# Optimization experiments

Hardware: AMD Instinct MI355X
Metric: run time of the kernel (lower is better)

## Reference

```python
import jax, jax.numpy as jnp
import numpy as np


def setup_inputs() -> dict:
    key = jax.random.key(0)
    k1, k2 = jax.random.split(key)
    num_tokens, top_k, num_experts = 1048576, 8, 64
    top_scores = jax.random.uniform(k1, (num_tokens, top_k), dtype=jnp.float32)
    selected_experts_indices = jax.random.randint(
        k2, (num_tokens, top_k), 0, num_experts, dtype=jnp.int64
    ) if jax.config.jax_enable_x64 else jax.random.randint(
        k2, (num_tokens, top_k), 0, num_experts, dtype=jnp.int32
    )
    return {
        "top_scores": top_scores,
        "selected_experts_indices": selected_experts_indices,
        "num_experts": num_experts,
    }


def reference(top_scores, selected_experts_indices, num_experts):
    flat_idx = selected_experts_indices.reshape(-1)  # [num_tokens*top_k]
    # histogram of tokens per expert (torch.histc returns float)
    num_tokens_per_expert = jnp.bincount(flat_idx, length=num_experts).astype(jnp.float32)
    # stable argsort by expert id -> permutation grouping tokens by expert
    token_indices_experts_sorted = jnp.argsort(flat_idx, stable=True)
    # gather routing scores into expert-sorted order
    top_scores_experts_sorted = top_scores.reshape(-1)[token_indices_experts_sorted]
    return (
        top_scores_experts_sorted,
        token_indices_experts_sorted,
        num_tokens_per_expert,
    )
```

## Files before the change

### kernel.cpp

```cpp
#include <hip/hip_runtime.h>


#define TILE 2048
#define WCH  512
#define RND  8

__device__ __forceinline__ unsigned long long match_mask(
    unsigned key,
    unsigned long long b0, unsigned long long b1, unsigned long long b2,
    unsigned long long b3, unsigned long long b4, unsigned long long b5,
    unsigned long long am) {
  unsigned long long m = am;
  m &= (key & 1u)  ? b0 : ~b0;
  m &= (key & 2u)  ? b1 : ~b1;
  m &= (key & 4u)  ? b2 : ~b2;
  m &= (key & 8u)  ? b3 : ~b3;
  m &= (key & 16u) ? b4 : ~b4;
  m &= (key & 32u) ? b5 : ~b5;
  return m;
}

__global__ __launch_bounds__(256) void hist_kernel(
    const int* __restrict__ idx, unsigned* __restrict__ countsT,
    int N, int nb) {
  __shared__ unsigned h[4][64];
  const int wave = threadIdx.x >> 6;
  const int lane = threadIdx.x & 63;

  long long base = (long long)blockIdx.x * TILE;
  long long rem = (long long)N - base;
  unsigned cnt = 0;

  if (rem >= TILE) {
    const int4* v = (const int4*)(idx + base);
    int4 x0 = v[threadIdx.x];
    int4 x1 = v[threadIdx.x + 256];
    unsigned es[8] = {
        ((unsigned)x0.x) & 63u, ((unsigned)x0.y) & 63u,
        ((unsigned)x0.z) & 63u, ((unsigned)x0.w) & 63u,
        ((unsigned)x1.x) & 63u, ((unsigned)x1.y) & 63u,
        ((unsigned)x1.z) & 63u, ((unsigned)x1.w) & 63u};
    #pragma unroll
    for (int r = 0; r < 8; ++r) {
      unsigned e = es[r];
      unsigned long long b0 = __ballot(e & 1u);
      unsigned long long b1 = __ballot(e & 2u);
      unsigned long long b2 = __ballot(e & 4u);
      unsigned long long b3 = __ballot(e & 8u);
      unsigned long long b4 = __ballot(e & 16u);
      unsigned long long b5 = __ballot(e & 32u);
      cnt += (unsigned)__popcll(
          match_mask((unsigned)lane, b0, b1, b2, b3, b4, b5, ~0ull));
    }
  } else {
    long long wstart = base + (long long)wave * WCH;
    for (int r = 0; r < RND; ++r) {
      long long i = wstart + (long long)r * 64 + lane;
      bool valid = i < (long long)N;
      unsigned long long am = __ballot(valid ? 1 : 0);
      unsigned e = valid ? (((unsigned)idx[i]) & 63u) : 0u;
      unsigned long long b0 = __ballot(e & 1u);
      unsigned long long b1 = __ballot(e & 2u);
      unsigned long long b2 = __ballot(e & 4u);
      unsigned long long b3 = __ballot(e & 8u);
      unsigned long long b4 = __ballot(e & 16u);
      unsigned long long b5 = __ballot(e & 32u);
      cnt += (unsigned)__popcll(
          match_mask((unsigned)lane, b0, b1, b2, b3, b4, b5, am));
    }
  }

  h[wave][lane] = cnt;
  __syncthreads();
  if (threadIdx.x < 64) {
    countsT[(size_t)blockIdx.x * 64 + threadIdx.x] =
        h[0][threadIdx.x] + h[1][threadIdx.x] + h[2][threadIdx.x] + h[3][threadIdx.x];
  }
}

__global__ __launch_bounds__(256) void scan_kernel(
    unsigned* __restrict__ countsT, unsigned* __restrict__ totals,
    float* __restrict__ out_counts, int nb) {
  int e = blockIdx.x;
  int t = threadIdx.x;
  int per = (nb + 255) >> 8;
  int base = t * per;

  unsigned s = 0;
  for (int j = 0; j < per; ++j) {
    int w = base + j;
    if (w < nb) s += countsT[(size_t)w * 64 + e];
  }
  __shared__ unsigned sh[256];
  sh[t] = s;
  __syncthreads();
  for (int d = 1; d < 256; d <<= 1) {
    unsigned v = sh[t];
    unsigned a = (t >= d) ? sh[t - d] : 0u;
    __syncthreads();
    sh[t] = v + a;
    __syncthreads();
  }
  unsigned incl = sh[t];
  unsigned run = incl - s;
  for (int j = 0; j < per; ++j) {
    int w = base + j;
    if (w < nb) {
      unsigned v = countsT[(size_t)w * 64 + e];
      countsT[(size_t)w * 64 + e] = run;
      run += v;
    }
  }
  if (t == 255) {
    totals[e] = incl;
    out_counts[e] = (float)incl;
  }
}

__global__ __launch_bounds__(256, 8) void scatter_kernel(
    const int* __restrict__ idx, const float* __restrict__ scores,
    const unsigned* __restrict__ baseT, const unsigned* __restrict__ totals,
    float* __restrict__ out_scores, float* __restrict__ out_idx,
    int N, int nb) {
  __shared__ uint2    sdat[TILE];
  __shared__ unsigned shc[4][64];
  __shared__ unsigned gdest[64];

  const int wave = threadIdx.x >> 6;
  const int lane = threadIdx.x & 63;
  const unsigned long long lt = (1ull << lane) - 1ull;

  const long long start = (long long)blockIdx.x * TILE + (long long)wave * WCH;
  const bool fullt = ((long long)(blockIdx.x + 1) * TILE) <= (long long)N;

  const unsigned tot = totals[lane];
  const unsigned gb0 = baseT[(size_t)blockIdx.x * 64 + lane];

  unsigned e_pk[2] = {0, 0};
  unsigned r_pk[2] = {0, 0};
  unsigned c_pk[2] = {0, 0};
  float    sreg[RND];
  unsigned wtotal = 0;

  if (fullt) {
    #pragma unroll
    for (int r = 0; r < RND; ++r) {
      long long i = start + r * 64 + lane;
      unsigned e = ((unsigned)idx[i]) & 63u;
      sreg[r] = scores[i];
      unsigned long long b0 = __ballot(e & 1u);
      unsigned long long b1 = __ballot(e & 2u);
      unsigned long long b2 = __ballot(e & 4u);
      unsigned long long b3 = __ballot(e & 8u);
      unsigned long long b4 = __ballot(e & 16u);
      unsigned long long b5 = __ballot(e & 32u);
      unsigned long long ms = match_mask(e, b0, b1, b2, b3, b4, b5, ~0ull);
      unsigned rank = (unsigned)__popcll(ms & lt);
      unsigned cnt  = (unsigned)__popcll(
          match_mask((unsigned)lane, b0, b1, b2, b3, b4, b5, ~0ull));
      const int q = r >> 2, sh = (r & 3) * 8;
      e_pk[q] |= e << sh;
      r_pk[q] |= rank << sh;
      c_pk[q] |= cnt << sh;
      wtotal += cnt;
    }
  } else {
    for (int j = threadIdx.x; j < TILE; j += 256) sdat[j].y = 0xFFFFFFFFu;
    __syncthreads();
    for (int r = 0; r < RND; ++r) {
      long long i = start + (long long)r * 64 + lane;
      bool valid = i < (long long)N;
      unsigned long long am = __ballot(valid ? 1 : 0);
      unsigned e = valid ? (((unsigned)idx[i]) & 63u) : 0u;
      sreg[r] = valid ? scores[i] : 0.0f;
      unsigned long long b0 = __ballot(e & 1u);
      unsigned long long b1 = __ballot(e & 2u);
      unsigned long long b2 = __ballot(e & 4u);
      unsigned long long b3 = __ballot(e & 8u);
      unsigned long long b4 = __ballot(e & 16u);
      unsigned long long b5 = __ballot(e & 32u);
      unsigned long long ms = match_mask(e, b0, b1, b2, b3, b4, b5, am);
      unsigned rank = (unsigned)__popcll(ms & lt);
      unsigned cnt  = (unsigned)__popcll(
          match_mask((unsigned)lane, b0, b1, b2, b3, b4, b5, am));
      const int q = r >> 2, sh = (r & 3) * 8;
      e_pk[q] |= e << sh;
      r_pk[q] |= rank << sh;
      c_pk[q] |= cnt << sh;
      wtotal += cnt;
    }
  }

  shc[wave][lane] = wtotal;
  __syncthreads();

  unsigned c0 = shc[0][lane], c1 = shc[1][lane];
  unsigned c2 = shc[2][lane], c3 = shc[3][lane];
  unsigned bt = c0 + c1 + c2 + c3;
  unsigned wpre = 0;
  if (wave > 0) wpre += c0;
  if (wave > 1) wpre += c1;
  if (wave > 2) wpre += c2;

  unsigned s = bt;
  #pragma unroll
  for (int d = 1; d < 64; d <<= 1) {
    unsigned nv = __shfl_up(s, d, 64);
    if (lane >= d) s += nv;
  }
  unsigned bstart = s - bt;
  unsigned wbase = bstart + wpre;

  unsigned cur[RND];
  {
    unsigned acc = wbase;
    #pragma unroll
    for (int r = 0; r < RND; ++r) {
      cur[r] = acc;
      acc += (c_pk[r >> 2] >> ((r & 3) * 8)) & 0xffu;
    }
  }

  if (wave == 0) {
    unsigned s2 = tot;
    #pragma unroll
    for (int d = 1; d < 64; d <<= 1) {
      unsigned nv = __shfl_up(s2, d, 64);
      if (lane >= d) s2 += nv;
    }
    unsigned estart = s2 - tot;
    gdest[lane] = estart + gb0 - bstart;
  }

  if (fullt) {
    #pragma unroll
    for (int r = 0; r < RND; ++r) {
      unsigned i32 = (unsigned)(start + r * 64 + lane);
      const int q = r >> 2, sh = (r & 3) * 8;
      unsigned e    = (e_pk[q] >> sh) & 0xffu;
      unsigned rank = (r_pk[q] >> sh) & 0xffu;
      unsigned pos = (unsigned)__shfl((int)cur[r], (int)e, 64) + rank;
      sdat[pos] = make_uint2(__float_as_uint(sreg[r]), (i32 << 6) | e);
    }
  } else {
    for (int r = 0; r < RND; ++r) {
      long long i = start + (long long)r * 64 + lane;
      bool valid = i < (long long)N;
      const int q = r >> 2, sh = (r & 3) * 8;
      unsigned e    = (e_pk[q] >> sh) & 0xffu;
      unsigned rank = (r_pk[q] >> sh) & 0xffu;
      unsigned pos = (unsigned)__shfl((int)cur[r], (int)e, 64) + rank;
      if (valid) {
        sdat[pos] = make_uint2(__float_as_uint(sreg[r]), (((unsigned)i) << 6) | e);
      }
    }
  }
  __syncthreads();

  if (fullt) {
    #pragma unroll
    for (int k = 0; k < TILE / 256; ++k) {
      int j = threadIdx.x + k * 256;
      uint2 v = sdat[j];
      unsigned e = v.y & 63u;
      unsigned d = gdest[e] + (unsigned)j;
      out_scores[d] = __uint_as_float(v.x);
      out_idx[d] = (float)(v.y >> 6);
    }
  } else {
    for (int j = threadIdx.x; j < TILE; j += 256) {
      uint2 v = sdat[j];
      if (v.y == 0xFFFFFFFFu) continue;
      unsigned e = v.y & 63u;
      unsigned d = gdest[e] + (unsigned)j;
      out_scores[d] = __uint_as_float(v.x);
      out_idx[d] = (float)(v.y >> 6);
    }
  }
}

extern "C" void kernel_launch(void* const* d_in, const int* in_sizes, int n_in,
                              void* d_out, int out_size, void* d_ws, size_t ws_size,
                              hipStream_t stream) {
  const float* scores = (const float*)d_in[0];
  const int* idx = (const int*)d_in[1];
  int N = in_sizes[0];

  float* out_scores = (float*)d_out;
  float* out_idx = out_scores + N;
  float* out_counts = out_idx + N;

  int nb = (N + TILE - 1) / TILE;
  unsigned* countsT = (unsigned*)d_ws;
  unsigned* totals = countsT + (size_t)nb * 64;

  hist_kernel<<<nb, 256, 0, stream>>>(idx, countsT, N, nb);
  scan_kernel<<<64, 256, 0, stream>>>(countsT, totals, out_counts, nb);
  scatter_kernel<<<nb, 256, 0, stream>>>(idx, scores, countsT, totals,
                                         out_scores, out_idx, N, nb);
}
```

Before: 151.8 us.

## Double tile size, transpose per-block count layout, rewrite scan with wave shuffles

Doubles the per-block tile to 4096 elements, which halves the number of blocks and the size of the count matrix. It also transposes the per-block expert counts to an expert-major layout, so the scan reads and writes each expert's row contiguously. The scan is rewritten as a chunked shared-memory scan using wave shuffles in place of the strided serial loops and barrier-heavy Hillis-Steele scan. In exchange, the scatter kernel holds twice as many registers per thread and shared memory per block, and its occupancy hint drops to 4 blocks per SM, which can reduce latency hiding.

```diff
diff --git a/kernel.cpp b/kernel.cpp
--- a/kernel.cpp
+++ b/kernel.cpp
@@ -1,9 +1,9 @@
 #include <hip/hip_runtime.h>
 
 
-#define TILE 2048
-#define WCH  512
-#define RND  8
+#define TILE 4096
+#define WCH  1024
+#define RND  16
 
 __device__ __forceinline__ unsigned long long match_mask(
     unsigned key,
@@ -33,15 +33,17 @@
 
   if (rem >= TILE) {
     const int4* v = (const int4*)(idx + base);
-    int4 x0 = v[threadIdx.x];
-    int4 x1 = v[threadIdx.x + 256];
-    unsigned es[8] = {
-        ((unsigned)x0.x) & 63u, ((unsigned)x0.y) & 63u,
-        ((unsigned)x0.z) & 63u, ((unsigned)x0.w) & 63u,
-        ((unsigned)x1.x) & 63u, ((unsigned)x1.y) & 63u,
-        ((unsigned)x1.z) & 63u, ((unsigned)x1.w) & 63u};
-    #pragma unroll
-    for (int r = 0; r < 8; ++r) {
+    unsigned es[16];
+    #pragma unroll
+    for (int k = 0; k < 4; ++k) {
+      int4 x = v[threadIdx.x + k * 256];
+      es[k * 4 + 0] = ((unsigned)x.x) & 63u;
+      es[k * 4 + 1] = ((unsigned)x.y) & 63u;
+      es[k * 4 + 2] = ((unsigned)x.z) & 63u;
+      es[k * 4 + 3] = ((unsigned)x.w) & 63u;
+    }
+    #pragma unroll
+    for (int r = 0; r < 16; ++r) {
       unsigned e = es[r];
       unsigned long long b0 = __ballot(e & 1u);
       unsigned long long b1 = __ballot(e & 2u);
@@ -73,7 +75,7 @@
   h[wave][lane] = cnt;
   __syncthreads();
   if (threadIdx.x < 64) {
-    countsT[(size_t)blockIdx.x * 64 + threadIdx.x] =
+    countsT[(size_t)threadIdx.x * nb + blockIdx.x] =
         h[0][threadIdx.x] + h[1][threadIdx.x] + h[2][threadIdx.x] + h[3][threadIdx.x];
   }
 }
@@ -81,43 +83,49 @@
 __global__ __launch_bounds__(256) void scan_kernel(
     unsigned* __restrict__ countsT, unsigned* __restrict__ totals,
     float* __restrict__ out_counts, int nb) {
-  int e = blockIdx.x;
-  int t = threadIdx.x;
-  int per = (nb + 255) >> 8;
-  int base = t * per;
-
-  unsigned s = 0;
-  for (int j = 0; j < per; ++j) {
-    int w = base + j;
-    if (w < nb) s += countsT[(size_t)w * 64 + e];
-  }
-  __shared__ unsigned sh[256];
-  sh[t] = s;
-  __syncthreads();
-  for (int d = 1; d < 256; d <<= 1) {
-    unsigned v = sh[t];
-    unsigned a = (t >= d) ? sh[t - d] : 0u;
-    __syncthreads();
-    sh[t] = v + a;
-    __syncthreads();
-  }
-  unsigned incl = sh[t];
-  unsigned run = incl - s;
-  for (int j = 0; j < per; ++j) {
-    int w = base + j;
-    if (w < nb) {
-      unsigned v = countsT[(size_t)w * 64 + e];
-      countsT[(size_t)w * 64 + e] = run;
-      run += v;
-    }
-  }
-  if (t == 255) {
-    totals[e] = incl;
-    out_counts[e] = (float)incl;
-  }
-}
-
-__global__ __launch_bounds__(256, 8) void scatter_kernel(
+  const int e = blockIdx.x;
+  const int t = threadIdx.x;
+  const int wave = t >> 6;
+  const int lane = t & 63;
+  unsigned* row = countsT + (size_t)e * nb;
+
+  __shared__ unsigned buf[2048];
+  __shared__ unsigned wsum[4];
+
+  unsigned carry = 0;
+  for (int c = 0; c < nb; c += 2048) {
+    int m = nb - c; if (m > 2048) m = 2048;
+    for (int j = t; j < 2048; j += 256) buf[j] = (j < m) ? row[c + j] : 0u;
+    __syncthreads();
+    unsigned v[8]; unsigned s = 0;
+    #pragma unroll
+    for (int k = 0; k < 8; ++k) { v[k] = buf[t * 8 + k]; s += v[k]; }
+    unsigned inc = s;
+    #pragma unroll
+    for (int d = 1; d < 64; d <<= 1) {
+      unsigned nv = __shfl_up(inc, d, 64);
+      if (lane >= d) inc += nv;
+    }
+    if (lane == 63) wsum[wave] = inc;
+    __syncthreads();
+    unsigned woff = 0;
+    for (int w = 0; w < wave; ++w) woff += wsum[w];
+    unsigned btot = wsum[0] + wsum[1] + wsum[2] + wsum[3];
+    unsigned run = carry + woff + (inc - s);
+    #pragma unroll
+    for (int k = 0; k < 8; ++k) { buf[t * 8 + k] = run; run += v[k]; }
+    __syncthreads();
+    for (int j = t; j < 2048; j += 256) if (j < m) row[c + j] = buf[j];
+    carry += btot;
+    __syncthreads();
+  }
+  if (t == 0) {
+    totals[e] = carry;
+    out_counts[e] = (float)carry;
+  }
+}
+
+__global__ __launch_bounds__(256, 4) void scatter_kernel(
     const int* __restrict__ idx, const float* __restrict__ scores,
     const unsigned* __restrict__ baseT, const unsigned* __restrict__ totals,
     float* __restrict__ out_scores, float* __restrict__ out_idx,
@@ -134,11 +142,11 @@
   const bool fullt = ((long long)(blockIdx.x + 1) * TILE) <= (long long)N;
 
   const unsigned tot = totals[lane];
-  const unsigned gb0 = baseT[(size_t)blockIdx.x * 64 + lane];
-
-  unsigned e_pk[2] = {0, 0};
-  unsigned r_pk[2] = {0, 0};
-  unsigned c_pk[2] = {0, 0};
+  const unsigned gb0 = baseT[(size_t)lane * nb + blockIdx.x];
+
+  unsigned e_pk[4] = {0, 0, 0, 0};
+  unsigned r_pk[4] = {0, 0, 0, 0};
+  unsigned c_pk[4] = {0, 0, 0, 0};
   float    sreg[RND];
   unsigned wtotal = 0;
 
@@ -292,7 +300,7 @@
 
   int nb = (N + TILE - 1) / TILE;
   unsigned* countsT = (unsigned*)d_ws;
-  unsigned* totals = countsT + (size_t)nb * 64;
+  unsigned* totals = countsT + (size_t)64 * nb;
 
   hist_kernel<<<nb, 256, 0, stream>>>(idx, countsT, N, nb);
   scan_kernel<<<64, 256, 0, stream>>>(countsT, totals, out_counts, nb);
```

Result: faster. 142.5 us (-6.2%).
